# Performance work log

Measured on AMD Instinct MI355X. Metric: run time of the kernel, lower is better.

## Reference

```python
import jax, jax.numpy as jnp
import numpy as np

B, S, D = 2, 4096, 2048
H = 16
DC = 512       # dim_c
DKQV = 2048    # dim_kqv
DR = 1024      # dim_r
DCKV = 512     # dim_c_kv
DOUT = 2048
DH = DKQV // H   # 128
DRH = DR // H    # 64
SCALER = 1.0 / float(np.sqrt(DH + DRH))


def _rope(x):
    # x: [B, S, H, DRH]; rotation indexed by sequence position (axis 1)
    dr = x.shape[-1]
    inv_freq = 1.0 / (10000.0 ** (jnp.arange(0, dr, 2, dtype=jnp.float32) / dr))
    t = jnp.arange(x.shape[1], dtype=jnp.float32)
    freqs = t[:, None] * inv_freq[None, :]            # [S, dr/2]
    emb = jnp.concatenate([freqs, freqs], axis=-1)[None, :, None, :]  # [1,S,1,dr]
    x1, x2 = jnp.split(x, 2, axis=-1)
    rot = jnp.concatenate([-x2, x1], axis=-1)
    return x * jnp.cos(emb) + rot * jnp.sin(emb)


def setup_inputs() -> dict:
    key = jax.random.key(0)
    ks = jax.random.split(key, 20)
    def lin(k, din, dout):
        s = 1.0 / np.sqrt(din)
        kw, kb = jax.random.split(k)
        W = jax.random.uniform(kw, (din, dout), jnp.float32, -s, s)
        b = jax.random.uniform(kb, (dout,), jnp.float32, -s, s)
        return W, b
    h_t = jax.random.normal(ks[0], (B, S, D), jnp.float32)
    Wc, bc = lin(ks[1], D, DC)
    Wcq, bcq = lin(ks[2], DC, DKQV)
    Wqr, bqr = lin(ks[3], DC, DR)
    Wckv, bckv = lin(ks[4], D, DCKV)
    Wck, bck = lin(ks[5], DCKV, DKQV)
    Wkr, bkr = lin(ks[6], D, DR)
    Wv, bv = lin(ks[7], DCKV, DKQV)
    Wo, bo = lin(ks[8], DKQV, DOUT)
    return dict(h_t=h_t, Wc=Wc, bc=bc, Wcq=Wcq, bcq=bcq, Wqr=Wqr, bqr=bqr,
                Wckv=Wckv, bckv=bckv, Wck=Wck, bck=bck, Wkr=Wkr, bkr=bkr,
                Wv=Wv, bv=bv, Wo=Wo, bo=bo)


def reference(h_t, Wc, bc, Wcq, bcq, Wqr, bqr, Wckv, bckv, Wck, bck,
              Wkr, bkr, Wv, bv, Wo, bo):
    b, s = h_t.shape[0], h_t.shape[1]
    cq = h_t @ Wc + bc                                   # [B,S,DC]
    q = (cq @ Wcq + bcq).reshape(b, s, H, DH)            # [B,S,H,DH]
    qr = _rope((cq @ Wqr + bqr).reshape(b, s, H, DRH))   # [B,S,H,DRH]
    q = jnp.concatenate([q, qr], axis=-1)                # [B,S,H,DH+DRH]
    ckv = h_t @ Wckv + bckv                              # [B,S,DCKV]
    k = (ckv @ Wck + bck).reshape(b, s, H, DH)
    kr = _rope((h_t @ Wkr + bkr).reshape(b, s, H, DRH))
    k = jnp.concatenate([k, kr], axis=-1)
    v = (ckv @ Wv + bv).reshape(b, s, H, DH)
    # Faithful to source: matmul over last two dims of [B,S,H,d] ->
    # per-position head-vs-head scores [B,S,H,H], softmax over heads.
    scores = jnp.einsum('bsid,bsjd->bsij', q, k) * SCALER
    attn = jax.nn.softmax(scores, axis=-1)
    out = jnp.einsum('bsij,bsjd->bsid', attn, v).reshape(b, s, DKQV)
    return out @ Wo + bo
```

## Files before the change

### kernel.cpp

```cpp
#include <hip/hip_runtime.h>
#include <hip/hip_bf16.h>
#include <stdint.h>


typedef __bf16 bf16_t;
typedef __bf16 bf16x8 __attribute__((ext_vector_type(8)));
typedef float f32x4 __attribute__((ext_vector_type(4)));

__device__ __forceinline__ void async_copy16(const void* g, void* l) {
  __builtin_amdgcn_global_load_lds(
      (__attribute__((address_space(1))) void*)(void*)g,
      (__attribute__((address_space(3))) void*)l, 16, 0, 0);
}

template <typename OT>
__global__ __launch_bounds__(256) void gemm_bt(
    const bf16_t* __restrict__ A, long lda,
    const bf16_t* __restrict__ BT,
    const float* __restrict__ bias,
    OT* __restrict__ C, long ldc,
    int M, int N, int K)
{
  __shared__ __align__(16) bf16_t As[128 * 64];
  __shared__ __align__(16) bf16_t Bs[128 * 64];

  const int tid  = threadIdx.x;
  const int lane = tid & 63;
  const int w    = tid >> 6;
  const int wm   = w >> 1, wn = w & 1;
  const int quad = lane >> 4, r16 = lane & 15;
  const long row0 = (long)blockIdx.y * 128;
  const long col0 = (long)blockIdx.x * 128;

  f32x4 acc[4][4];
#pragma unroll
  for (int i = 0; i < 4; i++)
#pragma unroll
    for (int j = 0; j < 4; j++)
      acc[i][j] = (f32x4){0.f, 0.f, 0.f, 0.f};

  for (int k0 = 0; k0 < K; k0 += 64) {
#pragma unroll
    for (int p = 0; p < 4; p++) {
      const int idx = p * 256 + tid;
      const int rr  = idx >> 3;
      const int cg  = ((idx & 7) ^ (rr & 7)) * 8;
      async_copy16(A  + (row0 + rr) * lda + k0 + cg, As + (p * 256 + w * 64) * 8);
      async_copy16(BT + (col0 + rr) * (long)K + k0 + cg, Bs + (p * 256 + w * 64) * 8);
    }
    __syncthreads();

#pragma unroll
    for (int kk = 0; kk < 64; kk += 32) {
      const int kc = kk >> 3;
      bf16x8 av[4], bv[4];
#pragma unroll
      for (int i = 0; i < 4; i++) {
        const int ra = wm * 64 + i * 16 + r16;
        av[i] = *(const bf16x8*)(As + ra * 64 + (((kc + quad) ^ (ra & 7)) * 8));
      }
#pragma unroll
      for (int j = 0; j < 4; j++) {
        const int rb = wn * 64 + j * 16 + r16;
        bv[j] = *(const bf16x8*)(Bs + rb * 64 + (((kc + quad) ^ (rb & 7)) * 8));
      }
#pragma unroll
      for (int i = 0; i < 4; i++)
#pragma unroll
        for (int j = 0; j < 4; j++)
          acc[i][j] = __builtin_amdgcn_mfma_f32_16x16x32_bf16(av[i], bv[j], acc[i][j], 0, 0, 0);
    }
    __syncthreads();
  }

#pragma unroll
  for (int j = 0; j < 4; j++) {
    const long col = col0 + wn * 64 + j * 16 + r16;
    const float bj = bias[col];
#pragma unroll
    for (int i = 0; i < 4; i++) {
      const long row = row0 + wm * 64 + i * 16 + quad * 4;
#pragma unroll
      for (int rr = 0; rr < 4; rr++)
        C[(row + rr) * ldc + col] = (OT)(acc[i][j][rr] + bj);
    }
  }
}

__global__ void transpose_f32_bf16(const float* __restrict__ in, bf16_t* __restrict__ out,
                                   int R, int C)
{
  __shared__ bf16_t tile[32][33];
  const int cb = blockIdx.x * 32, rb = blockIdx.y * 32;
  const int tx = threadIdx.x, ty = threadIdx.y;
#pragma unroll
  for (int i = 0; i < 32; i += 8)
    tile[ty + i][tx] = (bf16_t)in[(size_t)(rb + ty + i) * C + cb + tx];
  __syncthreads();
#pragma unroll
  for (int i = 0; i < 32; i += 8)
    out[(size_t)(cb + ty + i) * R + rb + tx] = tile[tx][ty + i];
}

__global__ void cvt_f32_bf16(const float* __restrict__ in, bf16_t* __restrict__ out, long n)
{
  const long i = ((long)blockIdx.x * blockDim.x + threadIdx.x) * 8;
  if (i >= n) return;
  const float4 a = *(const float4*)(in + i);
  const float4 b = *(const float4*)(in + i + 4);
  bf16x8 o;
  o[0] = (bf16_t)a.x; o[1] = (bf16_t)a.y; o[2] = (bf16_t)a.z; o[3] = (bf16_t)a.w;
  o[4] = (bf16_t)b.x; o[5] = (bf16_t)b.y; o[6] = (bf16_t)b.z; o[7] = (bf16_t)b.w;
  *(bf16x8*)(out + i) = o;
}

__global__ void concat_bias(const float* bc, const float* bckv, const float* bkr,
                            const float* bcq, const float* bqr,
                            const float* bck, const float* bv,
                            float* b1, float* b2, float* b3)
{
  const int t = blockIdx.x * 256 + threadIdx.x;
  if (t < 2048) {
    b1[t] = (t < 512) ? bc[t] : (t < 1024) ? bckv[t - 512] : bkr[t - 1024];
  } else if (t < 5120) {
    const int u = t - 2048;
    b2[u] = (u < 2048) ? bcq[u] : bqr[u - 2048];
  } else if (t < 9216) {
    const int u = t - 5120;
    b3[u] = (u < 2048) ? bck[u] : bv[u - 2048];
  }
}

__global__ __launch_bounds__(256) void attn_rope(
    const bf16_t* __restrict__ f1, bf16_t* f2, const bf16_t* __restrict__ f3)
{
  const int tok = blockIdx.x;
  const int pos = tok & 4095;
  const int tid = threadIdx.x;

  __shared__ __align__(16) float qf[16 * 204];
  __shared__ __align__(16) float kf[16 * 204];
  __shared__ __align__(16) float vf[16 * 132];
  __shared__ float sc[256];

  const bf16_t* q  = f2 + (size_t)tok * 3072;
  const bf16_t* qr = q + 2048;
  const bf16_t* k  = f3 + (size_t)tok * 4096;
  const bf16_t* v  = k + 2048;
  const bf16_t* kr = f1 + (size_t)tok * 2048 + 1024;

  {
    const int h = tid >> 4, d = (tid & 15) * 8;
    bf16x8 xq = *(const bf16x8*)(q + tid * 8);
    bf16x8 xk = *(const bf16x8*)(k + tid * 8);
    bf16x8 xv = *(const bf16x8*)(v + tid * 8);
    float* qd = qf + h * 204 + d;
    float* kd = kf + h * 204 + d;
    float* vd = vf + h * 132 + d;
#pragma unroll
    for (int e = 0; e < 8; e++) {
      qd[e] = (float)xq[e];
      kd[e] = (float)xk[e];
      vd[e] = (float)xv[e];
    }
  }

  for (int p = tid; p < 512; p += 256) {
    const int h = p >> 5, j = p & 31;
    const float x1 = (float)qr[h * 64 + j];
    const float x2 = (float)qr[h * 64 + j + 32];
    const float y1 = (float)kr[h * 64 + j];
    const float y2 = (float)kr[h * 64 + j + 32];
    const float ang = (float)pos * exp2f((float)j * -0.41524101186092029f);
    float sn, cs;
    sincosf(ang, &sn, &cs);
    qf[h * 204 + 128 + j] = x1 * cs - x2 * sn;
    qf[h * 204 + 160 + j] = x2 * cs + x1 * sn;
    kf[h * 204 + 128 + j] = y1 * cs - y2 * sn;
    kf[h * 204 + 160 + j] = y2 * cs + y1 * sn;
  }
  __syncthreads();

  {
    const int i = tid >> 4, j = tid & 15;
    const float4* qrow = (const float4*)(qf + i * 204);
    const float4* krow = (const float4*)(kf + j * 204);
    float d0 = 0.f, d1 = 0.f, d2 = 0.f, d3 = 0.f;
#pragma unroll 8
    for (int dd = 0; dd < 48; dd++) {
      const float4 a = qrow[dd], b = krow[dd];
      d0 = fmaf(a.x, b.x, d0);
      d1 = fmaf(a.y, b.y, d1);
      d2 = fmaf(a.z, b.z, d2);
      d3 = fmaf(a.w, b.w, d3);
    }
    const float s = (d0 + d1 + d2 + d3) * 0.07216878364870323f;
    float m = s;
    m = fmaxf(m, __shfl_xor(m, 1));
    m = fmaxf(m, __shfl_xor(m, 2));
    m = fmaxf(m, __shfl_xor(m, 4));
    m = fmaxf(m, __shfl_xor(m, 8));
    const float e = __expf(s - m);
    float sum = e;
    sum += __shfl_xor(sum, 1);
    sum += __shfl_xor(sum, 2);
    sum += __shfl_xor(sum, 4);
    sum += __shfl_xor(sum, 8);
    sc[i * 16 + j] = e / sum;
  }
  __syncthreads();

  {
    const int i = tid >> 4, dp = (tid & 15) * 8;
    float4 a0 = {0.f, 0.f, 0.f, 0.f}, a1 = {0.f, 0.f, 0.f, 0.f};
#pragma unroll
    for (int j = 0; j < 16; j++) {
      const float a = sc[i * 16 + j];
      const float4* vrow = (const float4*)(vf + j * 132 + dp);
      const float4 v0 = vrow[0], v1 = vrow[1];
      a0.x = fmaf(a, v0.x, a0.x);
      a0.y = fmaf(a, v0.y, a0.y);
      a0.z = fmaf(a, v0.z, a0.z);
      a0.w = fmaf(a, v0.w, a0.w);
      a1.x = fmaf(a, v1.x, a1.x);
      a1.y = fmaf(a, v1.y, a1.y);
      a1.z = fmaf(a, v1.z, a1.z);
      a1.w = fmaf(a, v1.w, a1.w);
    }
    bf16x8 o;
    o[0] = (bf16_t)a0.x; o[1] = (bf16_t)a0.y; o[2] = (bf16_t)a0.z; o[3] = (bf16_t)a0.w;
    o[4] = (bf16_t)a1.x; o[5] = (bf16_t)a1.y; o[6] = (bf16_t)a1.z; o[7] = (bf16_t)a1.w;
    *(bf16x8*)(f2 + (size_t)tok * 3072 + i * 128 + dp) = o;
  }
}

extern "C" void kernel_launch(void* const* d_in, const int* in_sizes, int n_in,
                              void* d_out, int out_size, void* d_ws, size_t ws_size,
                              hipStream_t stream)
{
  (void)in_sizes; (void)n_in; (void)out_size; (void)ws_size;

  const float* h_t  = (const float*)d_in[0];
  const float* Wc   = (const float*)d_in[1];
  const float* bc   = (const float*)d_in[2];
  const float* Wcq  = (const float*)d_in[3];
  const float* bcq  = (const float*)d_in[4];
  const float* Wqr  = (const float*)d_in[5];
  const float* bqr  = (const float*)d_in[6];
  const float* Wckv = (const float*)d_in[7];
  const float* bckv = (const float*)d_in[8];
  const float* Wck  = (const float*)d_in[9];
  const float* bck  = (const float*)d_in[10];
  const float* Wkr  = (const float*)d_in[11];
  const float* bkr  = (const float*)d_in[12];
  const float* Wv   = (const float*)d_in[13];
  const float* bv   = (const float*)d_in[14];
  const float* Wo   = (const float*)d_in[15];
  const float* bo   = (const float*)d_in[16];

  bf16_t* ws = (bf16_t*)d_ws;
  bf16_t* W1T    = ws + 0;
  bf16_t* W2T    = ws + 4194304;
  bf16_t* W3T    = ws + 5767168;
  bf16_t* WoT    = ws + 7864320;
  bf16_t* fused1 = ws + 12058624;
  bf16_t* fused2 = ws + 28835840;
  bf16_t* fused3 = ws + 54001664;

  bf16_t* hbf = (bf16_t*)d_out;
  float*  b1  = (float*)((char*)d_out + 33554432);
  float*  b2  = b1 + 2048;
  float*  b3  = b2 + 3072;

  const dim3 tb(32, 8);
  transpose_f32_bf16<<<dim3(16, 64), tb, 0, stream>>>(Wc,   W1T,                2048, 512);
  transpose_f32_bf16<<<dim3(16, 64), tb, 0, stream>>>(Wckv, W1T + 512  * 2048,  2048, 512);
  transpose_f32_bf16<<<dim3(32, 64), tb, 0, stream>>>(Wkr,  W1T + 1024 * 2048,  2048, 1024);
  transpose_f32_bf16<<<dim3(64, 16), tb, 0, stream>>>(Wcq,  W2T,                512, 2048);
  transpose_f32_bf16<<<dim3(32, 16), tb, 0, stream>>>(Wqr,  W2T + 2048 * 512,   512, 1024);
  transpose_f32_bf16<<<dim3(64, 16), tb, 0, stream>>>(Wck,  W3T,                512, 2048);
  transpose_f32_bf16<<<dim3(64, 16), tb, 0, stream>>>(Wv,   W3T + 2048 * 512,   512, 2048);
  transpose_f32_bf16<<<dim3(64, 64), tb, 0, stream>>>(Wo,   WoT,                2048, 2048);
  concat_bias<<<36, 256, 0, stream>>>(bc, bckv, bkr, bcq, bqr, bck, bv, b1, b2, b3);
  cvt_f32_bf16<<<8192, 256, 0, stream>>>(h_t, hbf, 16777216L);

  gemm_bt<bf16_t><<<dim3(16, 64), 256, 0, stream>>>(hbf, 2048, W1T, b1, fused1, 2048, 8192, 2048, 2048);
  gemm_bt<bf16_t><<<dim3(24, 64), 256, 0, stream>>>(fused1, 2048, W2T, b2, fused2, 3072, 8192, 3072, 512);
  gemm_bt<bf16_t><<<dim3(32, 64), 256, 0, stream>>>(fused1 + 512, 2048, W3T, b3, fused3, 4096, 8192, 4096, 512);

  attn_rope<<<8192, 256, 0, stream>>>(fused1, fused2, fused3);

  gemm_bt<float><<<dim3(16, 64), 256, 0, stream>>>(fused2, 3072, WoT, bo, (float*)d_out, 2048, 8192, 2048, 2048);
}
```

Measured before the change: 506.1 us.

## Replace GEMM with 256x256-tile, 4-stage async-prefetch pipelined kernel

Replaces the 128x128 single-buffered GEMM with a 256x256 tile kernel using 512 threads and a 4-deep LDS ring buffer for 32-wide K slices. Global-to-LDS loads are issued several iterations ahead, and MFMA phases are interleaved with explicit barriers, waitcnt and setprio, so memory latency overlaps compute and each loaded tile is reused more. The bf16 output path stages results through LDS for vectorized 16-byte stores. The cost is 128KB of LDS per block, large accumulator register pressure, and fewer blocks for the smaller GEMMs.

```diff
diff --git a/kernel.cpp b/kernel.cpp
--- a/kernel.cpp
+++ b/kernel.cpp
@@ -14,75 +14,154 @@
 }
 
 template <typename OT>
-__global__ __launch_bounds__(256) void gemm_bt(
+__global__ __launch_bounds__(512, 2) void gemm_bt256(
     const bf16_t* __restrict__ A, long lda,
     const bf16_t* __restrict__ BT,
     const float* __restrict__ bias,
     OT* __restrict__ C, long ldc,
     int M, int N, int K)
 {
-  __shared__ __align__(16) bf16_t As[128 * 64];
-  __shared__ __align__(16) bf16_t Bs[128 * 64];
+  __shared__ __align__(16) bf16_t As[4][8192];
+  __shared__ __align__(16) bf16_t Bs[4][8192];
 
   const int tid  = threadIdx.x;
   const int lane = tid & 63;
   const int w    = tid >> 6;
-  const int wm   = w >> 1, wn = w & 1;
+  const int wm   = w >> 2, wn = w & 3;
   const int quad = lane >> 4, r16 = lane & 15;
-  const long row0 = (long)blockIdx.y * 128;
-  const long col0 = (long)blockIdx.x * 128;
-
-  f32x4 acc[4][4];
-#pragma unroll
-  for (int i = 0; i < 4; i++)
+  const long row0 = (long)blockIdx.y * 256;
+  const long col0 = (long)blockIdx.x * 256;
+  const int NT = K >> 5;
+
+  const int rr0 = tid >> 2;
+  const int cg0 = (((tid & 3) ^ (rr0 & 3)) << 3);
+
+  f32x4 acc[8][4];
+#pragma unroll
+  for (int i = 0; i < 8; i++)
 #pragma unroll
     for (int j = 0; j < 4; j++)
       acc[i][j] = (f32x4){0.f, 0.f, 0.f, 0.f};
 
-  for (int k0 = 0; k0 < K; k0 += 64) {
-#pragma unroll
-    for (int p = 0; p < 4; p++) {
-      const int idx = p * 256 + tid;
-      const int rr  = idx >> 3;
-      const int cg  = ((idx & 7) ^ (rr & 7)) * 8;
-      async_copy16(A  + (row0 + rr) * lda + k0 + cg, As + (p * 256 + w * 64) * 8);
-      async_copy16(BT + (col0 + rr) * (long)K + k0 + cg, Bs + (p * 256 + w * 64) * 8);
-    }
-    __syncthreads();
-
-#pragma unroll
-    for (int kk = 0; kk < 64; kk += 32) {
-      const int kc = kk >> 3;
-      bf16x8 av[4], bv[4];
-#pragma unroll
-      for (int i = 0; i < 4; i++) {
-        const int ra = wm * 64 + i * 16 + r16;
-        av[i] = *(const bf16x8*)(As + ra * 64 + (((kc + quad) ^ (ra & 7)) * 8));
+#pragma unroll
+  for (int t = 0; t < 3; t++) {
+    const long kk = (long)((t < NT) ? t : NT - 1) << 5;
+    const long ga = (row0 + rr0) * lda + kk + cg0;
+    const long gb = (col0 + rr0) * (long)K + kk + cg0;
+    async_copy16(A  + ga,                  &As[t][w * 512]);
+    async_copy16(BT + gb,                  &Bs[t][w * 512]);
+    async_copy16(A  + ga + 128 * lda,      &As[t][4096 + w * 512]);
+    async_copy16(BT + gb + 128 * (long)K,  &Bs[t][4096 + w * 512]);
+  }
+  asm volatile("s_waitcnt vmcnt(8)" ::: "memory");
+  __builtin_amdgcn_s_barrier();
+
+  for (int t = 0; t < NT; t++) {
+    const bf16_t* as = &As[t & 3][0];
+    const bf16_t* bs = &Bs[t & 3][0];
+    bf16_t* pa = &As[(t + 3) & 3][0];
+    bf16_t* pb = &Bs[(t + 3) & 3][0];
+    const int  pt  = ((t + 3) < NT) ? (t + 3) : NT - 1;
+    const long pkk = (long)pt << 5;
+    const long ga = (row0 + rr0) * lda + pkk + cg0;
+    const long gb = (col0 + rr0) * (long)K + pkk + cg0;
+
+    bf16x8 av[4], bv[4];
+
+#pragma unroll
+    for (int i = 0; i < 4; i++) {
+      const int ra = wm * 128 + i * 16 + r16;
+      av[i] = *(const bf16x8*)(as + ra * 32 + ((quad ^ (ra & 3)) << 3));
+    }
+#pragma unroll
+    for (int j = 0; j < 4; j++) {
+      const int rb = wn * 64 + j * 16 + r16;
+      bv[j] = *(const bf16x8*)(bs + rb * 32 + ((quad ^ (rb & 3)) << 3));
+    }
+    async_copy16(A  + ga, pa + w * 512);
+    async_copy16(BT + gb, pb + w * 512);
+    asm volatile("" ::: "memory");
+    __builtin_amdgcn_s_barrier();
+    asm volatile("s_waitcnt lgkmcnt(0)" ::: "memory");
+    __builtin_amdgcn_sched_barrier(0);
+    __builtin_amdgcn_s_setprio(1);
+#pragma unroll
+    for (int i = 0; i < 4; i++)
+#pragma unroll
+      for (int j = 0; j < 4; j++)
+        acc[i][j] = __builtin_amdgcn_mfma_f32_16x16x32_bf16(av[i], bv[j], acc[i][j], 0, 0, 0);
+    __builtin_amdgcn_s_setprio(0);
+    __builtin_amdgcn_sched_barrier(0);
+    asm volatile("" ::: "memory");
+    __builtin_amdgcn_s_barrier();
+
+#pragma unroll
+    for (int i = 0; i < 4; i++) {
+      const int ra = wm * 128 + 64 + i * 16 + r16;
+      av[i] = *(const bf16x8*)(as + ra * 32 + ((quad ^ (ra & 3)) << 3));
+    }
+    async_copy16(A  + ga + 128 * lda,     pa + 4096 + w * 512);
+    async_copy16(BT + gb + 128 * (long)K, pb + 4096 + w * 512);
+    asm volatile("" ::: "memory");
+    __builtin_amdgcn_s_barrier();
+    asm volatile("s_waitcnt lgkmcnt(0)" ::: "memory");
+    __builtin_amdgcn_sched_barrier(0);
+    __builtin_amdgcn_s_setprio(1);
+#pragma unroll
+    for (int i = 0; i < 4; i++)
+#pragma unroll
+      for (int j = 0; j < 4; j++)
+        acc[i + 4][j] = __builtin_amdgcn_mfma_f32_16x16x32_bf16(av[i], bv[j], acc[i + 4][j], 0, 0, 0);
+    __builtin_amdgcn_s_setprio(0);
+    asm volatile("s_waitcnt vmcnt(8)" ::: "memory");
+    __builtin_amdgcn_sched_barrier(0);
+    asm volatile("" ::: "memory");
+    __builtin_amdgcn_s_barrier();
+  }
+
+#pragma unroll
+  for (int j = 0; j < 4; j++) {
+    const float bj = bias[col0 + wn * 64 + j * 16 + r16];
+#pragma unroll
+    for (int i = 0; i < 8; i++) {
+      acc[i][j][0] += bj; acc[i][j][1] += bj;
+      acc[i][j][2] += bj; acc[i][j][3] += bj;
+    }
+  }
+
+  if constexpr (sizeof(OT) == 2) {
+    asm volatile("s_waitcnt vmcnt(0)" ::: "memory");
+    __builtin_amdgcn_s_barrier();
+    bf16_t* wreg = (w < 4) ? &As[w][0] : &Bs[w - 4][0];
+#pragma unroll
+    for (int i = 0; i < 8; i++)
+#pragma unroll
+      for (int j = 0; j < 4; j++)
+#pragma unroll
+        for (int r = 0; r < 4; r++)
+          wreg[(i * 16 + quad * 4 + r) * 64 + j * 16 + r16] = (bf16_t)acc[i][j][r];
+    asm volatile("s_waitcnt lgkmcnt(0)" ::: "memory");
+    __builtin_amdgcn_s_barrier();
+#pragma unroll
+    for (int it = 0; it < 16; it++) {
+      const int r = it * 16 + (tid >> 5);
+      const int c = (tid & 31) * 8;
+      const int ww = ((r >> 7) << 2) + (c >> 6);
+      const bf16_t* src = ((ww < 4) ? &As[ww][0] : &Bs[ww - 4][0])
+                          + (r & 127) * 64 + (c & 63);
+      *(bf16x8*)((bf16_t*)C + (row0 + r) * ldc + col0 + c) = *(const bf16x8*)src;
+    }
+  } else {
+#pragma unroll
+    for (int j = 0; j < 4; j++) {
+      const long col = col0 + wn * 64 + j * 16 + r16;
+#pragma unroll
+      for (int i = 0; i < 8; i++) {
+        const long row = row0 + wm * 128 + i * 16 + quad * 4;
+#pragma unroll
+        for (int r = 0; r < 4; r++)
+          C[(row + r) * ldc + col] = (OT)acc[i][j][r];
       }
-#pragma unroll
-      for (int j = 0; j < 4; j++) {
-        const int rb = wn * 64 + j * 16 + r16;
-        bv[j] = *(const bf16x8*)(Bs + rb * 64 + (((kc + quad) ^ (rb & 7)) * 8));
-      }
-#pragma unroll
-      for (int i = 0; i < 4; i++)
-#pragma unroll
-        for (int j = 0; j < 4; j++)
-          acc[i][j] = __builtin_amdgcn_mfma_f32_16x16x32_bf16(av[i], bv[j], acc[i][j], 0, 0, 0);
-    }
-    __syncthreads();
-  }
-
-#pragma unroll
-  for (int j = 0; j < 4; j++) {
-    const long col = col0 + wn * 64 + j * 16 + r16;
-    const float bj = bias[col];
-#pragma unroll
-    for (int i = 0; i < 4; i++) {
-      const long row = row0 + wm * 64 + i * 16 + quad * 4;
-#pragma unroll
-      for (int rr = 0; rr < 4; rr++)
-        C[(row + rr) * ldc + col] = (OT)(acc[i][j][rr] + bj);
     }
   }
 }
@@ -284,11 +363,11 @@
   concat_bias<<<36, 256, 0, stream>>>(bc, bckv, bkr, bcq, bqr, bck, bv, b1, b2, b3);
   cvt_f32_bf16<<<8192, 256, 0, stream>>>(h_t, hbf, 16777216L);
 
-  gemm_bt<bf16_t><<<dim3(16, 64), 256, 0, stream>>>(hbf, 2048, W1T, b1, fused1, 2048, 8192, 2048, 2048);
-  gemm_bt<bf16_t><<<dim3(24, 64), 256, 0, stream>>>(fused1, 2048, W2T, b2, fused2, 3072, 8192, 3072, 512);
-  gemm_bt<bf16_t><<<dim3(32, 64), 256, 0, stream>>>(fused1 + 512, 2048, W3T, b3, fused3, 4096, 8192, 4096, 512);
+  gemm_bt256<bf16_t><<<dim3(8, 32), 512, 0, stream>>>(hbf, 2048, W1T, b1, fused1, 2048, 8192, 2048, 2048);
+  gemm_bt256<bf16_t><<<dim3(12, 32), 512, 0, stream>>>(fused1, 2048, W2T, b2, fused2, 3072, 8192, 3072, 512);
+  gemm_bt256<bf16_t><<<dim3(16, 32), 512, 0, stream>>>(fused1 + 512, 2048, W3T, b3, fused3, 4096, 8192, 4096, 512);
 
   attn_rope<<<8192, 256, 0, stream>>>(fused1, fused2, fused3);
 
-  gemm_bt<float><<<dim3(16, 64), 256, 0, stream>>>(fused2, 3072, WoT, bo, (float*)d_out, 2048, 8192, 2048, 2048);
-}
+  gemm_bt256<float><<<dim3(8, 32), 512, 0, stream>>>(fused2, 3072, WoT, bo, (float*)d_out, 2048, 8192, 2048, 2048);
+}
```

Result: no change. 505.6 us (-0.1%).

## Replace GEMM with 256x256 double-buffered pipelined 8-wave kernel

Applied to the files above, without the earlier changes.

Replaces the 128x128 single-buffered GEMM with a 256x256-tile, 512-thread kernel. It double-buffers LDS, interleaves async global-to-LDS loads with MFMA phases under barriers and priority hints, and remaps workgroup IDs for cache locality. The bf16 outputs are staged through LDS so stores are coalesced. This aims to hide memory latency and raise MFMA utilisation, at the cost of 128KB of LDS, a more fragile hand-tuned schedule and fewer workgroups per GEMM.

```diff
diff --git a/kernel.cpp b/kernel.cpp
--- a/kernel.cpp
+++ b/kernel.cpp
@@ -14,75 +14,155 @@
 }
 
 template <typename OT>
-__global__ __launch_bounds__(256) void gemm_bt(
+__global__ __launch_bounds__(512, 2) void gemm_bt256(
     const bf16_t* __restrict__ A, long lda,
     const bf16_t* __restrict__ BT,
     const float* __restrict__ bias,
     OT* __restrict__ C, long ldc,
     int M, int N, int K)
 {
-  __shared__ __align__(16) bf16_t As[128 * 64];
-  __shared__ __align__(16) bf16_t Bs[128 * 64];
+  __shared__ __align__(16) bf16_t As[2][16384];
+  __shared__ __align__(16) bf16_t Bs[2][16384];
 
   const int tid  = threadIdx.x;
   const int lane = tid & 63;
   const int w    = tid >> 6;
-  const int wm   = w >> 1, wn = w & 1;
+  const int wm   = w >> 2, wn = w & 3;
   const int quad = lane >> 4, r16 = lane & 15;
-  const long row0 = (long)blockIdx.y * 128;
-  const long col0 = (long)blockIdx.x * 128;
-
-  f32x4 acc[4][4];
-#pragma unroll
-  for (int i = 0; i < 4; i++)
+
+  const int nwg = gridDim.x * gridDim.y;
+  int wg = blockIdx.y * gridDim.x + blockIdx.x;
+  wg = (wg & 7) * (nwg >> 3) + (wg >> 3);
+  const int bx = wg % gridDim.x, by = wg / gridDim.x;
+  const long row0 = (long)by * 256;
+  const long col0 = (long)bx * 256;
+
+  const bf16_t* Ab = A + row0 * lda;
+  const bf16_t* Bb = BT + col0 * (long)K;
+
+  const int rdoff = r16 * 32 + ((quad * 8) ^ ((r16 & 8) ? 16 : 0));
+
+  const int srin = lane >> 2;
+  const int sksw = ((lane & 3) * 8) ^ ((lane & 32) ? 16 : 0);
+
+  const bf16_t* pA0 = Ab + (long)(w * 16 + srin) * lda + sksw;
+  const bf16_t* pA1 = Ab + (long)((8 + w) * 16 + srin) * lda + sksw;
+  const bf16_t* pB0 = Bb + (long)(w * 16 + srin) * K + sksw;
+  const bf16_t* pB1 = Bb + (long)((8 + w) * 16 + srin) * K + sksw;
+
+  f32x4 acc[8][4];
+#pragma unroll
+  for (int i = 0; i < 8; i++)
 #pragma unroll
     for (int j = 0; j < 4; j++)
       acc[i][j] = (f32x4){0.f, 0.f, 0.f, 0.f};
 
-  for (int k0 = 0; k0 < K; k0 += 64) {
-#pragma unroll
-    for (int p = 0; p < 4; p++) {
-      const int idx = p * 256 + tid;
-      const int rr  = idx >> 3;
-      const int cg  = ((idx & 7) ^ (rr & 7)) * 8;
-      async_copy16(A  + (row0 + rr) * lda + k0 + cg, As + (p * 256 + w * 64) * 8);
-      async_copy16(BT + (col0 + rr) * (long)K + k0 + cg, Bs + (p * 256 + w * 64) * 8);
-    }
+  bf16x8 av[4], bv[4];
+
+#define STA(koff, dbuf, Kc)                                                  \
+  async_copy16(pA0 + (koff) + (Kc) * 32, &As[dbuf][(w * 2 + (Kc)) << 9]);    \
+  async_copy16(pA1 + (koff) + (Kc) * 32, &As[dbuf][((8 + w) * 2 + (Kc)) << 9])
+#define STB(koff, dbuf, Kc)                                                  \
+  async_copy16(pB0 + (koff) + (Kc) * 32, &Bs[dbuf][(w * 2 + (Kc)) << 9]);    \
+  async_copy16(pB1 + (koff) + (Kc) * 32, &Bs[dbuf][((8 + w) * 2 + (Kc)) << 9])
+
+#define PHASE(RBUF, KH, MH, LOADB, STAGE_STMT, GATE)                         \
+  {                                                                          \
+    _Pragma("unroll")                                                        \
+    for (int i_ = 0; i_ < 4; i_++)                                           \
+      av[i_] = *(const bf16x8*)(&As[RBUF][0] +                               \
+                (((wm * 8 + (MH) * 4 + i_) * 2 + (KH)) << 9) + rdoff);       \
+    if (LOADB) {                                                             \
+      _Pragma("unroll")                                                      \
+      for (int j_ = 0; j_ < 4; j_++)                                         \
+        bv[j_] = *(const bf16x8*)(&Bs[RBUF][0] +                             \
+                  (((wn * 4 + j_) * 2 + (KH)) << 9) + rdoff);                \
+    }                                                                        \
+    STAGE_STMT;                                                              \
+    __builtin_amdgcn_s_barrier();                                            \
+    asm volatile("s_waitcnt lgkmcnt(0)" ::: "memory");                       \
+    __builtin_amdgcn_s_setprio(1);                                           \
+    _Pragma("unroll")                                                        \
+    for (int i_ = 0; i_ < 4; i_++)                                           \
+      _Pragma("unroll")                                                      \
+      for (int j_ = 0; j_ < 4; j_++)                                         \
+        acc[(MH) * 4 + i_][j_] = __builtin_amdgcn_mfma_f32_16x16x32_bf16(    \
+            av[i_], bv[j_], acc[(MH) * 4 + i_][j_], 0, 0, 0);                \
+    __builtin_amdgcn_s_setprio(0);                                           \
+    if (GATE) { asm volatile("s_waitcnt vmcnt(8)" ::: "memory"); }           \
+    __builtin_amdgcn_s_barrier();                                            \
+  }
+
+  STA(0, 0, 0);
+  STB(0, 0, 0);
+  STA(0, 0, 1);
+  STB(0, 0, 1);
+  STA(64, 1, 0);
+  STB(64, 1, 0);
+  asm volatile("s_waitcnt vmcnt(8)" ::: "memory");
+  __builtin_amdgcn_s_barrier();
+
+  const int NI = K >> 7;
+  for (int it = 0; it < NI; it++) {
+    PHASE(0, 0, 0, true,  STA(64, 1, 1),  false)
+    PHASE(0, 0, 1, false, STB(64, 1, 1),  true)
+    PHASE(0, 1, 0, true,  STA(128, 0, 0), false)
+    PHASE(0, 1, 1, false, STB(128, 0, 0), true)
+    PHASE(1, 0, 0, true,  STA(128, 0, 1), false)
+    PHASE(1, 0, 1, false, STB(128, 0, 1), true)
+    PHASE(1, 1, 0, true,  STA(192, 1, 0), false)
+    PHASE(1, 1, 1, false, STB(192, 1, 0), true)
+    pA0 += 128; pA1 += 128; pB0 += 128; pB1 += 128;
+  }
+#undef PHASE
+#undef STA
+#undef STB
+
+  asm volatile("s_waitcnt vmcnt(0)" ::: "memory");
+  __builtin_amdgcn_s_barrier();
+
+#pragma unroll
+  for (int j = 0; j < 4; j++) {
+    const float bj = bias[col0 + wn * 64 + j * 16 + r16];
+#pragma unroll
+    for (int i = 0; i < 8; i++) {
+      acc[i][j][0] += bj; acc[i][j][1] += bj;
+      acc[i][j][2] += bj; acc[i][j][3] += bj;
+    }
+  }
+
+  if constexpr (sizeof(OT) == 2) {
+    bf16_t* wreg = (w < 4) ? &As[w >> 1][(w & 1) * 8192]
+                           : &Bs[(w - 4) >> 1][((w - 4) & 1) * 8192];
+#pragma unroll
+    for (int i = 0; i < 8; i++)
+#pragma unroll
+      for (int j = 0; j < 4; j++)
+#pragma unroll
+        for (int r = 0; r < 4; r++)
+          wreg[(i * 16 + quad * 4 + r) * 64 + j * 16 + r16] = (bf16_t)acc[i][j][r];
     __syncthreads();
-
-#pragma unroll
-    for (int kk = 0; kk < 64; kk += 32) {
-      const int kc = kk >> 3;
-      bf16x8 av[4], bv[4];
-#pragma unroll
-      for (int i = 0; i < 4; i++) {
-        const int ra = wm * 64 + i * 16 + r16;
-        av[i] = *(const bf16x8*)(As + ra * 64 + (((kc + quad) ^ (ra & 7)) * 8));
+#pragma unroll
+    for (int itr = 0; itr < 16; itr++) {
+      const int r = itr * 16 + (tid >> 5);
+      const int c = (tid & 31) * 8;
+      const int ww = ((r >> 7) << 2) + (c >> 6);
+      const bf16_t* src = ((ww < 4) ? &As[ww >> 1][(ww & 1) * 8192]
+                                    : &Bs[(ww - 4) >> 1][((ww - 4) & 1) * 8192])
+                          + (r & 127) * 64 + (c & 63);
+      *(bf16x8*)((bf16_t*)C + (row0 + r) * ldc + col0 + c) = *(const bf16x8*)src;
+    }
+  } else {
+#pragma unroll
+    for (int j = 0; j < 4; j++) {
+      const long col = col0 + wn * 64 + j * 16 + r16;
+#pragma unroll
+      for (int i = 0; i < 8; i++) {
+        const long row = row0 + wm * 128 + i * 16 + quad * 4;
+#pragma unroll
+        for (int r = 0; r < 4; r++)
+          C[(row + r) * ldc + col] = (OT)acc[i][j][r];
       }
-#pragma unroll
-      for (int j = 0; j < 4; j++) {
-        const int rb = wn * 64 + j * 16 + r16;
-        bv[j] = *(const bf16x8*)(Bs + rb * 64 + (((kc + quad) ^ (rb & 7)) * 8));
-      }
-#pragma unroll
-      for (int i = 0; i < 4; i++)
-#pragma unroll
-        for (int j = 0; j < 4; j++)
-          acc[i][j] = __builtin_amdgcn_mfma_f32_16x16x32_bf16(av[i], bv[j], acc[i][j], 0, 0, 0);
-    }
-    __syncthreads();
-  }
-
-#pragma unroll
-  for (int j = 0; j < 4; j++) {
-    const long col = col0 + wn * 64 + j * 16 + r16;
-    const float bj = bias[col];
-#pragma unroll
-    for (int i = 0; i < 4; i++) {
-      const long row = row0 + wm * 64 + i * 16 + quad * 4;
-#pragma unroll
-      for (int rr = 0; rr < 4; rr++)
-        C[(row + rr) * ldc + col] = (OT)(acc[i][j][rr] + bj);
     }
   }
 }
@@ -284,11 +364,11 @@
   concat_bias<<<36, 256, 0, stream>>>(bc, bckv, bkr, bcq, bqr, bck, bv, b1, b2, b3);
   cvt_f32_bf16<<<8192, 256, 0, stream>>>(h_t, hbf, 16777216L);
 
-  gemm_bt<bf16_t><<<dim3(16, 64), 256, 0, stream>>>(hbf, 2048, W1T, b1, fused1, 2048, 8192, 2048, 2048);
-  gemm_bt<bf16_t><<<dim3(24, 64), 256, 0, stream>>>(fused1, 2048, W2T, b2, fused2, 3072, 8192, 3072, 512);
-  gemm_bt<bf16_t><<<dim3(32, 64), 256, 0, stream>>>(fused1 + 512, 2048, W3T, b3, fused3, 4096, 8192, 4096, 512);
+  gemm_bt256<bf16_t><<<dim3(8, 32), 512, 0, stream>>>(hbf, 2048, W1T, b1, fused1, 2048, 8192, 2048, 2048);
+  gemm_bt256<bf16_t><<<dim3(12, 32), 512, 0, stream>>>(fused1, 2048, W2T, b2, fused2, 3072, 8192, 3072, 512);
+  gemm_bt256<bf16_t><<<dim3(16, 32), 512, 0, stream>>>(fused1 + 512, 2048, W3T, b3, fused3, 4096, 8192, 4096, 512);
 
   attn_rope<<<8192, 256, 0, stream>>>(fused1, fused2, fused3);
 
-  gemm_bt<float><<<dim3(16, 64), 256, 0, stream>>>(fused2, 3072, WoT, bo, (float*)d_out, 2048, 8192, 2048, 2048);
-}
+  gemm_bt256<float><<<dim3(8, 32), 512, 0, stream>>>(fused2, 3072, WoT, bo, (float*)d_out, 2048, 8192, 2048, 2048);
+}
```

New measurement: 482.3 us. -4.7%, faster.
